# Performance work log

Measured on AMD Instinct MI355X. Metric: run time of the kernel, lower is better.

Reference implementation:

```python
import jax, jax.numpy as jnp
import numpy as np

# Quantization constants (from init_kwargs)
INPUT_SCALE = 0.05
OUTPUT_SCALE = 0.1
OUTPUT_ZERO_POINT = 0
FEATURE_BITWIDTH = 8
Q_MIN = -(1 << (FEATURE_BITWIDTH - 1))       # -128
Q_MAX = (1 << (FEATURE_BITWIDTH - 1)) - 1    #  127

B, IN_F, OUT_F = 8192, 4096, 4096


def setup_inputs() -> dict:
    key = jax.random.key(0)
    k_x, k_w, k_b, k_s = jax.random.split(key, 4)
    # int8 quantized activations and weights
    x = jax.random.randint(k_x, (B, IN_F), Q_MIN, Q_MAX + 1, dtype=jnp.int8)
    weight = jax.random.randint(k_w, (OUT_F, IN_F), Q_MIN, Q_MAX + 1, dtype=jnp.int8)
    # shifted quantized bias (int32)
    bias = jax.random.randint(k_b, (OUT_F,), -1000, 1000, dtype=jnp.int32)
    # per-output-channel weight scale (positive floats)
    weight_scale = jax.random.uniform(k_s, (OUT_F,), dtype=jnp.float32, minval=0.001, maxval=0.01)
    return {"x": x, "weight": weight, "bias": bias, "weight_scale": weight_scale}


def reference(x, weight, bias, weight_scale):
    # int32-accumulated GEMM: [B, in] @ [in, out] + bias -> [B, out]
    acc = jnp.matmul(x.astype(jnp.int32), weight.astype(jnp.int32).T,
                     preferred_element_type=jnp.int32) + bias[None, :]
    # dequant/requant epilogue with per-channel scale
    out = acc.astype(jnp.float32) * (INPUT_SCALE * weight_scale[None, :] / OUTPUT_SCALE) + OUTPUT_ZERO_POINT
    out = jnp.clip(jnp.round(out), Q_MIN, Q_MAX).astype(jnp.int8)
    return out
```

## Files before the change

### kernel.cpp

```cpp
#include <hip/hip_runtime.h>
#include <cstdint>
#include <cstddef>

#define M_DIM 8192
#define N_DIM 4096
#define K_DIM 4096

#define BM 128
#define BN 128
#define BK 64

using i32x4 = __attribute__((ext_vector_type(4))) int;

__device__ __forceinline__ void async_load16(const void* g, void* l) {
    __builtin_amdgcn_global_load_lds(
        (const __attribute__((address_space(1))) void*)g,
        (__attribute__((address_space(3))) void*)l,
        16, 0, 0);
}

__global__ __launch_bounds__(256) void pack_i8_kernel(const int4* __restrict__ src,
                                                      int* __restrict__ dst) {
    const long base = (long)blockIdx.x * 1024 + threadIdx.x;
#pragma unroll
    for (int j = 0; j < 4; ++j) {
        const long i = base + 256 * j;
        const int4 v = src[i];
        dst[i] = (v.x & 0xff) | ((v.y & 0xff) << 8) | ((v.z & 0xff) << 16) | (v.w << 24);
    }
}

__global__ __launch_bounds__(256) void qgemm_i8_kernel(const int8_t* __restrict__ A,
                                                       const int8_t* __restrict__ B,
                                                       const int* __restrict__ bias,
                                                       const float* __restrict__ wscale,
                                                       int* __restrict__ C) {
    __shared__ int8_t As[BM * BK];
    __shared__ int8_t Bs[BN * BK];

    const int tid  = threadIdx.x;
    const int wave = tid >> 6;
    const int lane = tid & 63;
    const int bm = blockIdx.y;
    const int bn = blockIdx.x;

    const int8_t* Ab = A + (size_t)bm * BM * K_DIM;
    const int8_t* Bb = B + (size_t)bn * BN * K_DIM;

    const int wm = wave >> 1;
    const int wn = wave & 1;

    i32x4 acc[4][4] = {};

    const int srow = lane >> 2;
    const int scol = (lane & 3) * 16;

    const int kq   = (lane >> 4) * 16;
    const int mrow = wm * 64 + (lane & 15);
    const int nrow = wn * 64 + (lane & 15);

    for (int kt = 0; kt < K_DIM; kt += BK) {
#pragma unroll
        for (int c = 0; c < 2; ++c) {
            const int rbase = (c * 4 + wave) * 16;
            async_load16(Ab + (size_t)(rbase + srow) * K_DIM + kt + scol,
                         &As[(c * 4 + wave) * 1024]);
            async_load16(Bb + (size_t)(rbase + srow) * K_DIM + kt + scol,
                         &Bs[(c * 4 + wave) * 1024]);
        }
        __syncthreads();

        i32x4 af[4], bf[4];
#pragma unroll
        for (int i = 0; i < 4; ++i)
            af[i] = *(const i32x4*)&As[(mrow + i * 16) * BK + kq];
#pragma unroll
        for (int j = 0; j < 4; ++j)
            bf[j] = *(const i32x4*)&Bs[(nrow + j * 16) * BK + kq];

#pragma unroll
        for (int i = 0; i < 4; ++i)
#pragma unroll
            for (int j = 0; j < 4; ++j)
                acc[i][j] = __builtin_amdgcn_mfma_i32_16x16x64_i8(af[i], bf[j], acc[i][j], 0, 0, 0);

        __syncthreads();
    }

    const int col16 = lane & 15;
    const int rquad = (lane >> 4) * 4;
#pragma unroll
    for (int j = 0; j < 4; ++j) {
        const int col = bn * BN + wn * 64 + j * 16 + col16;
        float s = 0.05f * wscale[col];
        s = s / 0.1f;
        const float bz = (float)bias[col];
#pragma unroll
        for (int i = 0; i < 4; ++i) {
            const int row0 = bm * BM + wm * 64 + i * 16 + rquad;
#pragma unroll
            for (int r = 0; r < 4; ++r) {
                float v = ((float)acc[i][j][r] + bz) * s;
                v = rintf(v);
                v = fminf(fmaxf(v, -128.0f), 127.0f);
                C[(size_t)(row0 + r) * N_DIM + col] = (int)v;
            }
        }
    }
}

extern "C" void kernel_launch(void* const* d_in, const int* in_sizes, int n_in,
                              void* d_out, int out_size, void* d_ws, size_t ws_size,
                              hipStream_t stream) {
    const int*   x32    = (const int*)d_in[0];
    const int*   w32    = (const int*)d_in[1];
    const int*   bias   = (const int*)d_in[2];
    const float* wscale = (const float*)d_in[3];
    int*         out    = (int*)d_out;

    int8_t* xp = (int8_t*)d_ws;
    int8_t* wp = xp + (size_t)M_DIM * K_DIM;

    {
        const int blocks = (int)((long)M_DIM * K_DIM / 4 / 1024);
        pack_i8_kernel<<<blocks, 256, 0, stream>>>((const int4*)x32, (int*)xp);
    }
    {
        const int blocks = (int)((long)N_DIM * K_DIM / 4 / 1024);
        pack_i8_kernel<<<blocks, 256, 0, stream>>>((const int4*)w32, (int*)wp);
    }

    dim3 grid(N_DIM / BN, M_DIM / BM);
    qgemm_i8_kernel<<<grid, 256, 0, stream>>>(xp, wp, bias, wscale, out);
}
```

Measured before the change: 422.2 us.

## Fuse int32-to-int8 packing into GEMM tile loads, dropping separate pack kernels

Removes the two standalone pack kernels. The GEMM now reads the int32-stored inputs directly, packs them to int8 in registers with byte-permute instructions, and writes them to shared memory. This removes the workspace round-trip and two extra launches. The cost is that the GEMM now streams four times as many bytes from global memory on every tile reload, since each tile is re-read by many blocks, and it drops the async global-to-LDS loads. The trailing barrier is also removed and the next tile's loads are issued before the first barrier.

Measured after the change: 679.5 us. +60.9%, slower.

```diff
diff --git a/kernel.cpp b/kernel.cpp
--- a/kernel.cpp
+++ b/kernel.cpp
@@ -12,29 +12,17 @@
 
 using i32x4 = __attribute__((ext_vector_type(4))) int;
 
-__device__ __forceinline__ void async_load16(const void* g, void* l) {
-    __builtin_amdgcn_global_load_lds(
-        (const __attribute__((address_space(1))) void*)g,
-        (__attribute__((address_space(3))) void*)l,
-        16, 0, 0);
+__device__ __forceinline__ int pack4(i32x4 v) {
+    unsigned t01 = __builtin_amdgcn_perm((unsigned)v.y, (unsigned)v.x, 0x00000400u);
+    unsigned t23 = __builtin_amdgcn_perm((unsigned)v.w, (unsigned)v.z, 0x00000400u);
+    return (int)__builtin_amdgcn_perm(t23, t01, 0x05040100u);
 }
 
-__global__ __launch_bounds__(256) void pack_i8_kernel(const int4* __restrict__ src,
-                                                      int* __restrict__ dst) {
-    const long base = (long)blockIdx.x * 1024 + threadIdx.x;
-#pragma unroll
-    for (int j = 0; j < 4; ++j) {
-        const long i = base + 256 * j;
-        const int4 v = src[i];
-        dst[i] = (v.x & 0xff) | ((v.y & 0xff) << 8) | ((v.z & 0xff) << 16) | (v.w << 24);
-    }
-}
-
-__global__ __launch_bounds__(256) void qgemm_i8_kernel(const int8_t* __restrict__ A,
-                                                       const int8_t* __restrict__ B,
-                                                       const int* __restrict__ bias,
-                                                       const float* __restrict__ wscale,
-                                                       int* __restrict__ C) {
+__global__ __launch_bounds__(256) void qgemm_fused_kernel(const int* __restrict__ A32,
+                                                          const int* __restrict__ B32,
+                                                          const int* __restrict__ bias,
+                                                          const float* __restrict__ wscale,
+                                                          int* __restrict__ C) {
     __shared__ int8_t As[BM * BK];
     __shared__ int8_t Bs[BN * BK];
 
@@ -44,29 +32,46 @@
     const int bm = blockIdx.y;
     const int bn = blockIdx.x;
 
-    const int8_t* Ab = A + (size_t)bm * BM * K_DIM;
-    const int8_t* Bb = B + (size_t)bn * BN * K_DIM;
-
     const int wm = wave >> 1;
     const int wn = wave & 1;
 
-    i32x4 acc[4][4] = {};
+    const int srow = wave * 4 + (lane >> 4);
+    const int sch  = lane & 15;
 
-    const int srow = lane >> 2;
-    const int scol = (lane & 3) * 16;
+    const int* Ag = A32 + (size_t)(bm * BM + srow) * K_DIM + sch * 4;
+    const int* Bg = B32 + (size_t)(bn * BN + srow) * K_DIM + sch * 4;
+
+    int* AsW = (int*)&As[srow * BK + sch * 4];
+    int* BsW = (int*)&Bs[srow * BK + sch * 4];
 
     const int kq   = (lane >> 4) * 16;
     const int mrow = wm * 64 + (lane & 15);
     const int nrow = wn * 64 + (lane & 15);
 
+    i32x4 acc[4][4] = {};
+
     for (int kt = 0; kt < K_DIM; kt += BK) {
+        i32x4 a0[4], b0[4], a1[4], b1[4];
 #pragma unroll
-        for (int c = 0; c < 2; ++c) {
-            const int rbase = (c * 4 + wave) * 16;
-            async_load16(Ab + (size_t)(rbase + srow) * K_DIM + kt + scol,
-                         &As[(c * 4 + wave) * 1024]);
-            async_load16(Bb + (size_t)(rbase + srow) * K_DIM + kt + scol,
-                         &Bs[(c * 4 + wave) * 1024]);
+        for (int it = 0; it < 4; ++it) {
+            a0[it] = *(const i32x4*)(Ag + (size_t)(it * 16) * K_DIM + kt);
+            b0[it] = *(const i32x4*)(Bg + (size_t)(it * 16) * K_DIM + kt);
+        }
+        __syncthreads();
+#pragma unroll
+        for (int it = 0; it < 4; ++it) {
+            a1[it] = *(const i32x4*)(Ag + (size_t)((it + 4) * 16) * K_DIM + kt);
+            b1[it] = *(const i32x4*)(Bg + (size_t)((it + 4) * 16) * K_DIM + kt);
+        }
+#pragma unroll
+        for (int it = 0; it < 4; ++it) {
+            AsW[it * (16 * BK / 4)] = pack4(a0[it]);
+            BsW[it * (16 * BK / 4)] = pack4(b0[it]);
+        }
+#pragma unroll
+        for (int it = 0; it < 4; ++it) {
+            AsW[(it + 4) * (16 * BK / 4)] = pack4(a1[it]);
+            BsW[(it + 4) * (16 * BK / 4)] = pack4(b1[it]);
         }
         __syncthreads();
 
@@ -83,8 +88,6 @@
 #pragma unroll
             for (int j = 0; j < 4; ++j)
                 acc[i][j] = __builtin_amdgcn_mfma_i32_16x16x64_i8(af[i], bf[j], acc[i][j], 0, 0, 0);
-
-        __syncthreads();
     }
 
     const int col16 = lane & 15;
@@ -118,18 +121,6 @@
     const float* wscale = (const float*)d_in[3];
     int*         out    = (int*)d_out;
 
-    int8_t* xp = (int8_t*)d_ws;
-    int8_t* wp = xp + (size_t)M_DIM * K_DIM;
-
-    {
-        const int blocks = (int)((long)M_DIM * K_DIM / 4 / 1024);
-        pack_i8_kernel<<<blocks, 256, 0, stream>>>((const int4*)x32, (int*)xp);
-    }
-    {
-        const int blocks = (int)((long)N_DIM * K_DIM / 4 / 1024);
-        pack_i8_kernel<<<blocks, 256, 0, stream>>>((const int4*)w32, (int*)wp);
-    }
-
     dim3 grid(N_DIM / BN, M_DIM / BM);
-    qgemm_i8_kernel<<<grid, 256, 0, stream>>>(xp, wp, bias, wscale, out);
+    qgemm_fused_kernel<<<grid, 256, 0, stream>>>(x32, w32, bias, wscale, out);
 }
```

## Switch to 32x32x32 int8 MFMA with XOR-swizzled LDS and merged pack launch

Applied to the files above, without the earlier changes.

Replaces the 16x16x64 int8 MFMA tiling with 32x32x32 MFMA, which halves the number of fragment loads per wave for the same tile. Global-to-LDS loads now use an XOR swizzle on the 16-byte column chunk to reduce LDS bank conflicts on fragment reads. The epilogue is remapped to the 32x32 accumulator layout. The two int8 pack launches are merged into one kernel launch to cut launch overhead.

Result: slower. 457.9 us (+8.5%).

```diff
diff --git a/kernel.cpp b/kernel.cpp
--- a/kernel.cpp
+++ b/kernel.cpp
@@ -10,7 +10,8 @@
 #define BN 128
 #define BK 64
 
-using i32x4 = __attribute__((ext_vector_type(4))) int;
+using i32x4  = __attribute__((ext_vector_type(4))) int;
+using i32x16 = __attribute__((ext_vector_type(16))) int;
 
 __device__ __forceinline__ void async_load16(const void* g, void* l) {
     __builtin_amdgcn_global_load_lds(
@@ -19,9 +20,16 @@
         16, 0, 0);
 }
 
-__global__ __launch_bounds__(256) void pack_i8_kernel(const int4* __restrict__ src,
-                                                      int* __restrict__ dst) {
-    const long base = (long)blockIdx.x * 1024 + threadIdx.x;
+__global__ __launch_bounds__(256) void pack_i8_kernel(const int4* __restrict__ xsrc,
+                                                      int* __restrict__ xdst,
+                                                      const int4* __restrict__ wsrc,
+                                                      int* __restrict__ wdst,
+                                                      int nxblocks) {
+    const bool isw = (int)blockIdx.x >= nxblocks;
+    const int4* src = isw ? wsrc : xsrc;
+    int*       dst  = isw ? wdst : xdst;
+    const long bb   = isw ? ((long)blockIdx.x - nxblocks) : (long)blockIdx.x;
+    const long base = bb * 1024 + threadIdx.x;
 #pragma unroll
     for (int j = 0; j < 4; ++j) {
         const long i = base + 256 * j;
@@ -50,60 +58,67 @@
     const int wm = wave >> 1;
     const int wn = wave & 1;
 
-    i32x4 acc[4][4] = {};
+    i32x16 acc[2][2] = {};
 
     const int srow = lane >> 2;
-    const int scol = (lane & 3) * 16;
+    const int sxor = ((lane & 3) ^ (srow & 3)) * 16;
 
-    const int kq   = (lane >> 4) * 16;
-    const int mrow = wm * 64 + (lane & 15);
-    const int nrow = wn * 64 + (lane & 15);
+    const int l31 = lane & 31;
+    const int khi = lane >> 5;
+    const int x3  = lane & 3;
+    const int arow = wm * 64 + l31;
+    const int brow = wn * 64 + l31;
 
     for (int kt = 0; kt < K_DIM; kt += BK) {
 #pragma unroll
         for (int c = 0; c < 2; ++c) {
             const int rbase = (c * 4 + wave) * 16;
-            async_load16(Ab + (size_t)(rbase + srow) * K_DIM + kt + scol,
+            async_load16(Ab + (size_t)(rbase + srow) * K_DIM + kt + sxor,
                          &As[(c * 4 + wave) * 1024]);
-            async_load16(Bb + (size_t)(rbase + srow) * K_DIM + kt + scol,
+            async_load16(Bb + (size_t)(rbase + srow) * K_DIM + kt + sxor,
                          &Bs[(c * 4 + wave) * 1024]);
         }
         __syncthreads();
 
-        i32x4 af[4], bf[4];
+        i32x4 af[2][2], bf[2][2];
 #pragma unroll
-        for (int i = 0; i < 4; ++i)
-            af[i] = *(const i32x4*)&As[(mrow + i * 16) * BK + kq];
+        for (int i = 0; i < 2; ++i)
 #pragma unroll
-        for (int j = 0; j < 4; ++j)
-            bf[j] = *(const i32x4*)&Bs[(nrow + j * 16) * BK + kq];
+            for (int kk = 0; kk < 2; ++kk) {
+                const int q = (kk << 1) | khi;
+                af[i][kk] = *(const i32x4*)&As[(arow + i * 32) * BK + ((q ^ x3) * 16)];
+                bf[i][kk] = *(const i32x4*)&Bs[(brow + i * 32) * BK + ((q ^ x3) * 16)];
+            }
 
 #pragma unroll
-        for (int i = 0; i < 4; ++i)
+        for (int i = 0; i < 2; ++i)
 #pragma unroll
-            for (int j = 0; j < 4; ++j)
-                acc[i][j] = __builtin_amdgcn_mfma_i32_16x16x64_i8(af[i], bf[j], acc[i][j], 0, 0, 0);
+            for (int j = 0; j < 2; ++j)
+#pragma unroll
+                for (int kk = 0; kk < 2; ++kk)
+                    acc[i][j] = __builtin_amdgcn_mfma_i32_32x32x32_i8(af[i][kk], bf[j][kk],
+                                                                      acc[i][j], 0, 0, 0);
 
         __syncthreads();
     }
 
-    const int col16 = lane & 15;
-    const int rquad = (lane >> 4) * 4;
+    const int lrow4 = khi * 4;
 #pragma unroll
-    for (int j = 0; j < 4; ++j) {
-        const int col = bn * BN + wn * 64 + j * 16 + col16;
+    for (int j = 0; j < 2; ++j) {
+        const int col = bn * BN + wn * 64 + j * 32 + l31;
         float s = 0.05f * wscale[col];
         s = s / 0.1f;
         const float bz = (float)bias[col];
 #pragma unroll
-        for (int i = 0; i < 4; ++i) {
-            const int row0 = bm * BM + wm * 64 + i * 16 + rquad;
+        for (int i = 0; i < 2; ++i) {
+            const int row0 = bm * BM + wm * 64 + i * 32 + lrow4;
 #pragma unroll
-            for (int r = 0; r < 4; ++r) {
+            for (int r = 0; r < 16; ++r) {
+                const int row = row0 + (r & 3) + 8 * (r >> 2);
                 float v = ((float)acc[i][j][r] + bz) * s;
                 v = rintf(v);
                 v = fminf(fmaxf(v, -128.0f), 127.0f);
-                C[(size_t)(row0 + r) * N_DIM + col] = (int)v;
+                C[(size_t)row * N_DIM + col] = (int)v;
             }
         }
     }
@@ -122,12 +137,10 @@
     int8_t* wp = xp + (size_t)M_DIM * K_DIM;
 
     {
-        const int blocks = (int)((long)M_DIM * K_DIM / 4 / 1024);
-        pack_i8_kernel<<<blocks, 256, 0, stream>>>((const int4*)x32, (int*)xp);
-    }
-    {
-        const int blocks = (int)((long)N_DIM * K_DIM / 4 / 1024);
-        pack_i8_kernel<<<blocks, 256, 0, stream>>>((const int4*)w32, (int*)wp);
+        const int nxblocks = (int)((long)M_DIM * K_DIM / 4 / 1024);
+        const int nwblocks = (int)((long)N_DIM * K_DIM / 4 / 1024);
+        pack_i8_kernel<<<nxblocks + nwblocks, 256, 0, stream>>>(
+            (const int4*)x32, (int*)xp, (const int4*)w32, (int*)wp, nxblocks);
     }
 
     dim3 grid(N_DIM / BN, M_DIM / BM);
```

## Double-buffer LDS tiles in int8 GEMM and fuse the two pack launches

Applied to the files above, without the earlier changes.

The GEMM main loop now uses two LDS buffers per operand. It issues the async global-to-LDS loads for the next K tile before running the MFMAs on the current tile, so memory latency overlaps with compute, and it drops one barrier per iteration. The two int8 pack kernels for activations and weights are merged into a single launch that picks its source by block index, saving one kernel launch. LDS use doubles, which may reduce occupancy.

Measured after the change: 437.2 us. +3.6%, slower.

```diff
diff --git a/kernel.cpp b/kernel.cpp
--- a/kernel.cpp
+++ b/kernel.cpp
@@ -19,9 +19,16 @@
         16, 0, 0);
 }
 
-__global__ __launch_bounds__(256) void pack_i8_kernel(const int4* __restrict__ src,
-                                                      int* __restrict__ dst) {
-    const long base = (long)blockIdx.x * 1024 + threadIdx.x;
+__global__ __launch_bounds__(256) void pack_i8_kernel(const int4* __restrict__ xsrc,
+                                                      int* __restrict__ xdst,
+                                                      const int4* __restrict__ wsrc,
+                                                      int* __restrict__ wdst,
+                                                      int nxblocks) {
+    const bool isw = (int)blockIdx.x >= nxblocks;
+    const int4* src = isw ? wsrc : xsrc;
+    int*       dst  = isw ? wdst : xdst;
+    const long bb   = isw ? ((long)blockIdx.x - nxblocks) : (long)blockIdx.x;
+    const long base = bb * 1024 + threadIdx.x;
 #pragma unroll
     for (int j = 0; j < 4; ++j) {
         const long i = base + 256 * j;
@@ -35,8 +42,8 @@
                                                        const int* __restrict__ bias,
                                                        const float* __restrict__ wscale,
                                                        int* __restrict__ C) {
-    __shared__ int8_t As[BM * BK];
-    __shared__ int8_t Bs[BN * BK];
+    __shared__ int8_t As[2][BM * BK];
+    __shared__ int8_t Bs[2][BN * BK];
 
     const int tid  = threadIdx.x;
     const int wave = tid >> 6;
@@ -59,24 +66,36 @@
     const int mrow = wm * 64 + (lane & 15);
     const int nrow = wn * 64 + (lane & 15);
 
+#pragma unroll
+    for (int c = 0; c < 2; ++c) {
+        const int rbase = (c * 4 + wave) * 16;
+        async_load16(Ab + (size_t)(rbase + srow) * K_DIM + 0 + scol,
+                     &As[0][(c * 4 + wave) * 1024]);
+        async_load16(Bb + (size_t)(rbase + srow) * K_DIM + 0 + scol,
+                     &Bs[0][(c * 4 + wave) * 1024]);
+    }
+    __syncthreads();
+
+    int cur = 0;
     for (int kt = 0; kt < K_DIM; kt += BK) {
+        if (kt + BK < K_DIM) {
 #pragma unroll
-        for (int c = 0; c < 2; ++c) {
-            const int rbase = (c * 4 + wave) * 16;
-            async_load16(Ab + (size_t)(rbase + srow) * K_DIM + kt + scol,
-                         &As[(c * 4 + wave) * 1024]);
-            async_load16(Bb + (size_t)(rbase + srow) * K_DIM + kt + scol,
-                         &Bs[(c * 4 + wave) * 1024]);
+            for (int c = 0; c < 2; ++c) {
+                const int rbase = (c * 4 + wave) * 16;
+                async_load16(Ab + (size_t)(rbase + srow) * K_DIM + (kt + BK) + scol,
+                             &As[cur ^ 1][(c * 4 + wave) * 1024]);
+                async_load16(Bb + (size_t)(rbase + srow) * K_DIM + (kt + BK) + scol,
+                             &Bs[cur ^ 1][(c * 4 + wave) * 1024]);
+            }
         }
-        __syncthreads();
 
         i32x4 af[4], bf[4];
 #pragma unroll
         for (int i = 0; i < 4; ++i)
-            af[i] = *(const i32x4*)&As[(mrow + i * 16) * BK + kq];
+            af[i] = *(const i32x4*)&As[cur][(mrow + i * 16) * BK + kq];
 #pragma unroll
         for (int j = 0; j < 4; ++j)
-            bf[j] = *(const i32x4*)&Bs[(nrow + j * 16) * BK + kq];
+            bf[j] = *(const i32x4*)&Bs[cur][(nrow + j * 16) * BK + kq];
 
 #pragma unroll
         for (int i = 0; i < 4; ++i)
@@ -85,6 +104,7 @@
                 acc[i][j] = __builtin_amdgcn_mfma_i32_16x16x64_i8(af[i], bf[j], acc[i][j], 0, 0, 0);
 
         __syncthreads();
+        cur ^= 1;
     }
 
     const int col16 = lane & 15;
@@ -122,12 +142,10 @@
     int8_t* wp = xp + (size_t)M_DIM * K_DIM;
 
     {
-        const int blocks = (int)((long)M_DIM * K_DIM / 4 / 1024);
-        pack_i8_kernel<<<blocks, 256, 0, stream>>>((const int4*)x32, (int*)xp);
-    }
-    {
-        const int blocks = (int)((long)N_DIM * K_DIM / 4 / 1024);
-        pack_i8_kernel<<<blocks, 256, 0, stream>>>((const int4*)w32, (int*)wp);
+        const int nxblocks = (int)((long)M_DIM * K_DIM / 4 / 1024);
+        const int nwblocks = (int)((long)N_DIM * K_DIM / 4 / 1024);
+        pack_i8_kernel<<<nxblocks + nwblocks, 256, 0, stream>>>(
+            (const int4*)x32, (int*)xp, (const int4*)w32, (int*)wp, nxblocks);
     }
 
     dim3 grid(N_DIM / BN, M_DIM / BM);
```
